# Kernel tuning notes

Hardware: AMD Instinct MI355X
Metric: run time of the kernel (lower is better)

## Reference

```python
import jax, jax.numpy as jnp
import numpy as np

DIM = 256      # in_channels == hidden_channels
INNER = 256    # heads * dim_head
HEADS = 4
DH = 64        # dim_head = hidden_channels // num_heads
EDGE_DIM = 512 # 2 * in_channels
FF = 1024      # 4 * dim ff expansion
DEPTH = 2
OUT = 1
N = 50000      # two stacked graphs of 25000 nodes
E = 100000
HALF = 25000


def setup_inputs() -> dict:
    key = jax.random.key(0)
    ks = iter(jax.random.split(key, 32))

    def lin(fan_in, fan_out):
        w = jax.random.normal(next(ks), (DEPTH, fan_in, fan_out), jnp.float32) * (1.0 / np.sqrt(fan_in))
        b = jnp.zeros((DEPTH, fan_out), jnp.float32)
        return w, b

    x = jax.random.normal(next(ks), (N, DIM), jnp.float32)
    edge_index = jax.random.randint(next(ks), (2, E), 0, HALF, dtype=jnp.int32)
    Wq, bq = lin(DIM, INNER)
    Wkv, bkv = lin(DIM, 2 * INNER)
    We, be = lin(EDGE_DIM, INNER)
    Wo, bo = lin(INNER, DIM)
    W1, b1 = lin(DIM, FF)
    W2, b2 = lin(FF, DIM)
    g_attn = jax.random.normal(next(ks), (DEPTH, 3 * DIM, 1), jnp.float32) * (1.0 / np.sqrt(3 * DIM))
    g_ff = jax.random.normal(next(ks), (DEPTH, 3 * DIM, 1), jnp.float32) * (1.0 / np.sqrt(3 * DIM))
    ln1_g = jnp.ones((DEPTH, DIM), jnp.float32); ln1_b = jnp.zeros((DEPTH, DIM), jnp.float32)
    ln2_g = jnp.ones((DEPTH, DIM), jnp.float32); ln2_b = jnp.zeros((DEPTH, DIM), jnp.float32)
    Wout = jax.random.normal(next(ks), (DIM, OUT), jnp.float32) * (1.0 / np.sqrt(DIM))
    bout = jnp.zeros((OUT,), jnp.float32)
    return dict(x=x, edge_index=edge_index, ln1_g=ln1_g, ln1_b=ln1_b, Wq=Wq, bq=bq,
                Wkv=Wkv, bkv=bkv, We=We, be=be, Wo=Wo, bo=bo, g_attn=g_attn,
                ln2_g=ln2_g, ln2_b=ln2_b, W1=W1, b1=b1, W2=W2, b2=b2, g_ff=g_ff,
                Wout=Wout, bout=bout)


def _layer_norm(x, g, b):
    mu = jnp.mean(x, axis=-1, keepdims=True)
    var = jnp.mean(jnp.square(x - mu), axis=-1, keepdims=True)
    return (x - mu) * jax.lax.rsqrt(var + 1e-5) * g + b


def _gated_residual(x, res, w):
    # gate = sigmoid(Linear_no_bias(cat(x, res, x - res)))
    gate = jax.nn.sigmoid(jnp.concatenate([x, res, x - res], axis=-1) @ w)  # [n,1]
    return x * gate + res * (1.0 - gate)


def _forward(x, edge_index, ln1_g, ln1_b, Wq, bq, Wkv, bkv, We, be, Wo, bo, g_attn,
             ln2_g, ln2_b, W1, b1, W2, b2, g_ff, Wout, bout):
    src, dst = edge_index[0], edge_index[1]
    # edge_attr = cat(x[src], x[dst]) as built in DeepGraphTransformer_mse.forward
    edge_attr = jnp.concatenate([x[src], x[dst]], axis=-1)  # [E, 2*DIM]
    nodes = x
    n = nodes.shape[0]
    scale = DH ** -0.5
    for l in range(DEPTH):
        xn = _layer_norm(nodes, ln1_g[l], ln1_b[l])
        q = xn @ Wq[l] + bq[l]                                   # [n, INNER]
        k, v = jnp.split(xn @ Wkv[l] + bkv[l], 2, axis=-1)       # [n, INNER] each
        e = edge_attr @ We[l] + be[l]                            # [E, INNER]
        qe = q[dst].reshape(-1, HEADS, DH)                       # [E,H,Dh]
        ke = (k[src] + e).reshape(-1, HEADS, DH)
        ve = (v[src] + e).reshape(-1, HEADS, DH)
        sim = jnp.einsum('ehd,ehd->eh', qe, ke) * scale          # [E,H]
        smax = jax.ops.segment_max(sim, dst, num_segments=n)     # [n,H] (-inf for empty)
        ez = jnp.exp(sim - smax[dst])
        denom = jax.ops.segment_sum(ez, dst, num_segments=n)
        attn = ez / denom[dst]                                   # softmax over incoming edges
        agg = jax.ops.segment_sum(attn[:, :, None] * ve, dst, num_segments=n)
        attn_out = agg.reshape(n, INNER) @ Wo[l] + bo[l]         # [n, DIM]
        nodes = _gated_residual(attn_out, nodes, g_attn[l])
        xn2 = _layer_norm(nodes, ln2_g[l], ln2_b[l])
        h = jax.nn.gelu(xn2 @ W1[l] + b1[l], approximate=False) @ W2[l] + b2[l]
        nodes = _gated_residual(h, nodes, g_ff[l])
    z = nodes @ Wout + bout                                      # [n, OUT]
    return z


def reference(x, edge_index, ln1_g, ln1_b, Wq, bq, Wkv, bkv, We, be, Wo, bo, g_attn,
              ln2_g, ln2_b, W1, b1, W2, b2, g_ff, Wout, bout):
    z = _forward(x, edge_index, ln1_g, ln1_b, Wq, bq, Wkv, bkv, We, be, Wo, bo, g_attn,
                 ln2_g, ln2_b, W1, b1, W2, b2, g_ff, Wout, bout)
    half = z.shape[0] // 2
    z_old, z_new = z[:half], z[half:]
    return (z_new.reshape(-1), z_old, z_new)
```

## Files before the change

kernel.cpp:

```cpp
#include <hip/hip_runtime.h>
#include <cmath>

#define N_NODES 50000
#define N_EDGES 100000
#define HALF_N  25000
#define DIM     256
#define NDEPTH  2
#define MAXDEG  64

#define WT_QKVE 0
#define WT_WO   524288
#define WT_W1   589824
#define WT_W2   851968
#define WT_LAYER 1114112

typedef __bf16 bf16;
typedef bf16 bf16x8 __attribute__((ext_vector_type(8)));
typedef bf16 bf16x4 __attribute__((ext_vector_type(4)));
typedef float f32x4 __attribute__((ext_vector_type(4)));

__device__ __forceinline__ float wave_sum(float v) {
  v += __shfl_xor(v, 1);
  v += __shfl_xor(v, 2);
  v += __shfl_xor(v, 4);
  v += __shfl_xor(v, 8);
  v += __shfl_xor(v, 16);
  v += __shfl_xor(v, 32);
  return v;
}

__global__ void ln0_kernel(const float* __restrict__ in, const float* __restrict__ g,
                           const float* __restrict__ b, bf16* __restrict__ A2) {
  int row = blockIdx.x * 4 + (threadIdx.x >> 6);
  if (row >= HALF_N) return;
  int lane = threadIdx.x & 63;
  float4 x = reinterpret_cast<const float4*>(in + (size_t)row * DIM)[lane];
  float mu = wave_sum(x.x + x.y + x.z + x.w) * (1.0f / DIM);
  float d0 = x.x - mu, d1 = x.y - mu, d2 = x.z - mu, d3 = x.w - mu;
  float var = wave_sum(d0*d0 + d1*d1 + d2*d2 + d3*d3) * (1.0f / DIM);
  float r = rsqrtf(var + 1e-5f);
  float4 gv = reinterpret_cast<const float4*>(g)[lane];
  float4 bv = reinterpret_cast<const float4*>(b)[lane];
  bf16x4 o;
  o[0] = (bf16)(d0 * r * gv.x + bv.x);
  o[1] = (bf16)(d1 * r * gv.y + bv.y);
  o[2] = (bf16)(d2 * r * gv.z + bv.z);
  o[3] = (bf16)(d3 * r * gv.w + bv.w);
  *reinterpret_cast<bf16x4*>(A2 + (size_t)row * 512 + lane * 4) = o;
}

template<int KK, int NJ>
__global__ __launch_bounds__(256) void gemm_nloop(
    const bf16* __restrict__ A, const bf16* __restrict__ Wp,
    const float* __restrict__ bias, bf16* __restrict__ C, int M) {
  __shared__ bf16x8 As[KK * 8];
  __shared__ bf16x8 Bs[1024];
  const int tid = threadIdx.x;
  const int lane = tid & 63, wv = tid >> 6;
  const int wr = wv >> 1, wc = wv & 1;
  const int lm = lane & 15, kb = (lane >> 4) & 3;
  const int row0 = blockIdx.x * 64;
#pragma unroll
  for (int i = 0; i < KK / 32; ++i) {
    int idx = tid + i * 256;
    int row = idx & 63, k8 = idx >> 6;
    int rga = row0 + row; if (rga >= M) rga = M - 1;
    As[idx] = *reinterpret_cast<const bf16x8*>(A + (size_t)rga * KK + k8 * 8);
  }
  const bf16x8* Wp8 = reinterpret_cast<const bf16x8*>(Wp);
  for (int jn = 0; jn < NJ; ++jn) {
    f32x4 acc[2][4] = {};
    for (int step = 0; step < KK / 64; ++step) {
      __syncthreads();
#pragma unroll
      for (int i = 0; i < 4; ++i) {
        int idx = tid + i * 256;
        Bs[idx] = Wp8[(size_t)jn * (KK * 16) + step * 1024 + idx];
      }
      __syncthreads();
#pragma unroll
      for (int ks = 0; ks < 2; ++ks) {
        bf16x8 af[2], bf[4];
#pragma unroll
        for (int mi = 0; mi < 2; ++mi)
          af[mi] = As[(step * 8 + ks * 4 + kb) * 64 + wr * 32 + mi * 16 + lm];
#pragma unroll
        for (int ni = 0; ni < 4; ++ni)
          bf[ni] = Bs[(ks * 4 + kb) * 128 + wc * 64 + ni * 16 + lm];
#pragma unroll
        for (int mi = 0; mi < 2; ++mi)
#pragma unroll
          for (int ni = 0; ni < 4; ++ni)
            acc[mi][ni] = __builtin_amdgcn_mfma_f32_16x16x32_bf16(af[mi], bf[ni], acc[mi][ni], 0, 0, 0);
      }
    }
    __syncthreads();
    bf16* Cs = (bf16*)Bs;
#pragma unroll
    for (int ni = 0; ni < 4; ++ni) {
      int c = wc * 64 + ni * 16 + lm;
      float bval = bias[jn * 128 + c];
#pragma unroll
      for (int mi = 0; mi < 2; ++mi)
#pragma unroll
        for (int e = 0; e < 4; ++e) {
          int r = wr * 32 + mi * 16 + kb * 4 + e;
          Cs[r * 128 + c] = (bf16)(acc[mi][ni][e] + bval);
        }
    }
    __syncthreads();
    bf16x8* C8 = reinterpret_cast<bf16x8*>(C);
    const bf16x8* Cs8 = (const bf16x8*)Bs;
#pragma unroll
    for (int i = 0; i < 4; ++i) {
      int idx = tid + i * 256;
      int row = idx >> 4, c8 = idx & 15;
      int grow = row0 + row;
      if (grow < M) C8[(size_t)grow * (NJ * 16) + jn * 16 + c8] = Cs8[row * 16 + c8];
    }
  }
}

__global__ __launch_bounds__(512) void ff_fused(
    const bf16* __restrict__ A, const bf16* __restrict__ W1p,
    const float* __restrict__ b1, const bf16* __restrict__ W2p,
    const float* __restrict__ b2, bf16* __restrict__ C, int M) {
  __shared__ bf16x8 Xs[2048];
  __shared__ bf16x8 Bs[2048];
  __shared__ bf16x8 Hs[1024];
  const int tid = threadIdx.x;
  const int lane = tid & 63, wv = tid >> 6;
  const int wr = wv >> 2, wc = wv & 3;
  const int lm = lane & 15, kb = (lane >> 4) & 3;
  const int row0 = blockIdx.x * 64;
#pragma unroll
  for (int i = 0; i < 4; ++i) {
    int idx = tid + i * 512;
    int row = idx & 63, k8 = idx >> 6;
    int rga = row0 + row; if (rga >= M) rga = M - 1;
    Xs[idx] = *reinterpret_cast<const bf16x8*>(A + (size_t)rga * 256 + k8 * 8);
  }
  const bf16x8* W1p8 = (const bf16x8*)W1p;
  const bf16x8* W2p8 = (const bf16x8*)W2p;
  f32x4 acc[2][4] = {};
  bf16* hsb = (bf16*)Hs;
  for (int j = 0; j < 8; ++j) {
    f32x4 acc1[2][2] = {};
#pragma unroll
    for (int half = 0; half < 2; ++half) {
      __syncthreads();
#pragma unroll
      for (int i = 0; i < 4; ++i) {
        int idx = tid + i * 512;
        Bs[idx] = W1p8[j * 4096 + half * 2048 + idx];
      }
      __syncthreads();
#pragma unroll
      for (int ks = 0; ks < 4; ++ks) {
        bf16x8 af[2], bf[2];
#pragma unroll
        for (int mi = 0; mi < 2; ++mi)
          af[mi] = Xs[(half * 16 + ks * 4 + kb) * 64 + wr * 32 + mi * 16 + lm];
#pragma unroll
        for (int ni = 0; ni < 2; ++ni)
          bf[ni] = Bs[(ks * 4 + kb) * 128 + wc * 32 + ni * 16 + lm];
#pragma unroll
        for (int mi = 0; mi < 2; ++mi)
#pragma unroll
          for (int ni = 0; ni < 2; ++ni)
            acc1[mi][ni] = __builtin_amdgcn_mfma_f32_16x16x32_bf16(af[mi], bf[ni], acc1[mi][ni], 0, 0, 0);
      }
    }
#pragma unroll
    for (int ni = 0; ni < 2; ++ni) {
      int c = wc * 32 + ni * 16 + lm;
      float bval = b1[j * 128 + c];
#pragma unroll
      for (int mi = 0; mi < 2; ++mi)
#pragma unroll
        for (int e = 0; e < 4; ++e) {
          int r = wr * 32 + mi * 16 + kb * 4 + e;
          float v = acc1[mi][ni][e] + bval;
          v = 0.5f * v * (1.0f + erff(v * 0.70710678118654752f));
          hsb[((c >> 3) * 64 + r) * 8 + (c & 7)] = (bf16)v;
        }
    }
#pragma unroll
    for (int h2 = 0; h2 < 2; ++h2) {
      __syncthreads();
#pragma unroll
      for (int i = 0; i < 4; ++i) {
        int idx = tid + i * 512;
        Bs[idx] = W2p8[j * 4096 + h2 * 2048 + idx];
      }
      __syncthreads();
#pragma unroll
      for (int ks = 0; ks < 2; ++ks) {
        bf16x8 af[2], bf[4];
#pragma unroll
        for (int mi = 0; mi < 2; ++mi)
          af[mi] = Hs[(h2 * 8 + ks * 4 + kb) * 64 + wr * 32 + mi * 16 + lm];
#pragma unroll
        for (int ni = 0; ni < 4; ++ni)
          bf[ni] = Bs[(ks * 4 + kb) * 256 + wc * 64 + ni * 16 + lm];
#pragma unroll
        for (int mi = 0; mi < 2; ++mi)
#pragma unroll
          for (int ni = 0; ni < 4; ++ni)
            acc[mi][ni] = __builtin_amdgcn_mfma_f32_16x16x32_bf16(af[mi], bf[ni], acc[mi][ni], 0, 0, 0);
      }
    }
  }
  __syncthreads();
  bf16* Cs = (bf16*)Bs;
#pragma unroll
  for (int ni = 0; ni < 4; ++ni) {
    int c = wc * 64 + ni * 16 + lm;
    float bval = b2[c];
#pragma unroll
    for (int mi = 0; mi < 2; ++mi)
#pragma unroll
      for (int e = 0; e < 4; ++e) {
        int r = wr * 32 + mi * 16 + kb * 4 + e;
        Cs[r * 256 + c] = (bf16)(acc[mi][ni][e] + bval);
      }
  }
  __syncthreads();
  bf16x8* C8 = (bf16x8*)C;
  const bf16x8* Cs8 = (const bf16x8*)Bs;
#pragma unroll
  for (int i = 0; i < 4; ++i) {
    int idx = tid + i * 512;
    int row = idx >> 5, c8 = idx & 31;
    int grow = row0 + row;
    if (grow < M) C8[(size_t)grow * 32 + c8] = Cs8[row * 32 + c8];
  }
}

__global__ void ell_build(const int* __restrict__ ei, int* __restrict__ deg,
                          int* __restrict__ ell) {
  int e = blockIdx.x * 256 + threadIdx.x;
  if (e >= N_EDGES) return;
  int s = ei[e], d = ei[N_EDGES + e];
  int pos = atomicAdd(&deg[d], 1);
  if (pos < MAXDEG) ell[d * MAXDEG + pos] = s;
}

__global__ void attn_gather(const int* __restrict__ deg, const int* __restrict__ ell,
                            const bf16* __restrict__ qkv, bf16* __restrict__ agg) {
  int d = blockIdx.x * 4 + (threadIdx.x >> 6);
  if (d >= HALF_N) return;
  int lane = threadIdx.x & 63;
  int cnt = deg[d]; if (cnt > MAXDEG) cnt = MAXDEG;
  const bf16* qr = qkv + (size_t)d * 1024;
  bf16x4 qb = *reinterpret_cast<const bf16x4*>(qr + lane * 4);
  float q0 = (float)qb[0], q1 = (float)qb[1], q2 = (float)qb[2], q3 = (float)qb[3];
  float m = -INFINITY, den = 0.0f, a0 = 0.0f, a1 = 0.0f, a2 = 0.0f, a3 = 0.0f;
  for (int i = 0; i < cnt; ++i) {
    int s = ell[d * MAXDEG + i];
    const bf16* kr = qkv + (size_t)s * 1024;
    bf16x4 kb4 = *reinterpret_cast<const bf16x4*>(kr + 256 + lane * 4);
    bf16x4 vb4 = *reinterpret_cast<const bf16x4*>(kr + 512 + lane * 4);
    float p = q0 * (float)kb4[0] + q1 * (float)kb4[1] +
              q2 * (float)kb4[2] + q3 * (float)kb4[3];
    p += __shfl_xor(p, 1); p += __shfl_xor(p, 2);
    p += __shfl_xor(p, 4); p += __shfl_xor(p, 8);
    float sim = p * 0.125f;
    float nm = fmaxf(m, sim);
    float sc = expf(m - nm);
    float w  = expf(sim - nm);
    den = den * sc + w;
    a0 = a0 * sc + w * (float)vb4[0];
    a1 = a1 * sc + w * (float)vb4[1];
    a2 = a2 * sc + w * (float)vb4[2];
    a3 = a3 * sc + w * (float)vb4[3];
    m = nm;
  }
  bf16x4 o;
  if (cnt > 0) {
    float inv = 1.0f / den;
    bf16x4 eb = *reinterpret_cast<const bf16x4*>(qr + 768 + lane * 4);
    o[0] = (bf16)(a0 * inv + (float)eb[0]);
    o[1] = (bf16)(a1 * inv + (float)eb[1]);
    o[2] = (bf16)(a2 * inv + (float)eb[2]);
    o[3] = (bf16)(a3 * inv + (float)eb[3]);
  } else {
    o[0] = (bf16)0.0f; o[1] = (bf16)0.0f; o[2] = (bf16)0.0f; o[3] = (bf16)0.0f;
  }
  *reinterpret_cast<bf16x4*>(agg + (size_t)d * DIM + lane * 4) = o;
}

template<int DO_LN, int DO_OUT>
__global__ void gr_ln(const bf16* __restrict__ xin, const float* __restrict__ fb,
                      float* __restrict__ nodes, const float* __restrict__ w,
                      const float* __restrict__ g, const float* __restrict__ b,
                      bf16* __restrict__ xn, int xn_stride, int ln_rows,
                      const float* __restrict__ Wout, const float* __restrict__ bout,
                      float* __restrict__ out, int rows, int xvr, int row_off) {
  int r = blockIdx.x * 4 + (threadIdx.x >> 6);
  if (r >= rows) return;
  int lane = threadIdx.x & 63;
  float x0, x1, x2, x3;
  if (r < xvr) {
    bf16x4 xb = *reinterpret_cast<const bf16x4*>(xin + (size_t)r * DIM + lane * 4);
    x0 = (float)xb[0]; x1 = (float)xb[1]; x2 = (float)xb[2]; x3 = (float)xb[3];
  } else {
    float4 f = reinterpret_cast<const float4*>(fb)[lane];
    x0 = f.x; x1 = f.y; x2 = f.z; x3 = f.w;
  }
  float4 rv = reinterpret_cast<const float4*>(nodes + (size_t)r * DIM)[lane];
  float4 w0 = reinterpret_cast<const float4*>(w)[lane];
  float4 w1 = reinterpret_cast<const float4*>(w + 256)[lane];
  float4 w2 = reinterpret_cast<const float4*>(w + 512)[lane];
  float p = x0 * (w0.x + w2.x) + rv.x * (w1.x - w2.x)
          + x1 * (w0.y + w2.y) + rv.y * (w1.y - w2.y)
          + x2 * (w0.z + w2.z) + rv.z * (w1.z - w2.z)
          + x3 * (w0.w + w2.w) + rv.w * (w1.w - w2.w);
  p = wave_sum(p);
  float gate = 1.0f / (1.0f + expf(-p));
  float n0 = x0 * gate + rv.x * (1.0f - gate);
  float n1 = x1 * gate + rv.y * (1.0f - gate);
  float n2 = x2 * gate + rv.z * (1.0f - gate);
  float n3 = x3 * gate + rv.w * (1.0f - gate);
  if (!DO_OUT) {
    float4 o; o.x = n0; o.y = n1; o.z = n2; o.w = n3;
    reinterpret_cast<float4*>(nodes + (size_t)r * DIM)[lane] = o;
  }
  if (DO_LN) {
    if (r < ln_rows) {
      float mu = wave_sum(n0 + n1 + n2 + n3) * (1.0f / DIM);
      float d0 = n0 - mu, d1 = n1 - mu, d2 = n2 - mu, d3 = n3 - mu;
      float var = wave_sum(d0*d0 + d1*d1 + d2*d2 + d3*d3) * (1.0f / DIM);
      float rs = rsqrtf(var + 1e-5f);
      float4 gv = reinterpret_cast<const float4*>(g)[lane];
      float4 bv = reinterpret_cast<const float4*>(b)[lane];
      bf16x4 o;
      o[0] = (bf16)(d0 * rs * gv.x + bv.x);
      o[1] = (bf16)(d1 * rs * gv.y + bv.y);
      o[2] = (bf16)(d2 * rs * gv.z + bv.z);
      o[3] = (bf16)(d3 * rs * gv.w + bv.w);
      *reinterpret_cast<bf16x4*>(xn + (size_t)r * xn_stride + lane * 4) = o;
    }
  }
  if (DO_OUT) {
    float4 wv = reinterpret_cast<const float4*>(Wout)[lane];
    float z = n0 * wv.x + n1 * wv.y + n2 * wv.z + n3 * wv.w;
    z = wave_sum(z);
    if (lane == 0) {
      z += bout[0];
      int gr = row_off + r;
      if (gr < HALF_N) {
        out[HALF_N + gr] = z;
      } else {
        int j = gr - HALF_N;
        out[j] = z;
        out[2 * HALF_N + j] = z;
      }
    }
  }
}

__global__ void prep_w(const float* __restrict__ Wq, const float* __restrict__ Wkv,
                       const float* __restrict__ We, const float* __restrict__ Wo,
                       const float* __restrict__ W1, const float* __restrict__ W2,
                       bf16* __restrict__ wt) {
  int idx = blockIdx.x * 256 + threadIdx.x;
  if (idx >= 2 * WT_LAYER) return;
  int l = idx / WT_LAYER, r = idx % WT_LAYER;
  float v;
  if (r < 524288) {
    int jn = r >> 16, t = r & 65535;
    int k8 = t >> 10, u = t & 1023, n = u >> 3, e = u & 7;
    int ncol = jn * 128 + n, k = k8 * 8 + e;
    if (ncol < 256) v = (k < 256) ? Wq[l * 65536 + k * 256 + ncol] : 0.0f;
    else if (ncol < 512) { int c = ncol - 256;
      v = (k < 256) ? Wkv[l * 131072 + k * 512 + c] : We[l * 131072 + (k - 256) * 256 + c]; }
    else if (ncol < 768) { int c = ncol - 512;
      v = (k < 256) ? Wkv[l * 131072 + k * 512 + 256 + c] : We[l * 131072 + (k - 256) * 256 + c]; }
    else { int c = ncol - 768;
      v = (k < 256) ? 0.0f : We[l * 131072 + k * 256 + c]; }
  } else if (r < 589824) {
    int rr = r - 524288;
    int jn = rr >> 15, t = rr & 32767;
    int k8 = t >> 10, u = t & 1023, n = u >> 3, e = u & 7;
    v = Wo[l * 65536 + (k8 * 8 + e) * 256 + jn * 128 + n];
  } else if (r < 851968) {
    int rr = r - 589824;
    int j = rr >> 15, t = rr & 32767;
    int k8 = t >> 10, u = t & 1023, n = u >> 3, e = u & 7;
    v = W1[l * 262144 + (k8 * 8 + e) * 1024 + j * 128 + n];
  } else {
    int rr = r - 851968;
    int j = rr >> 15, t = rr & 32767;
    int k8 = t >> 11, u = t & 2047, n = u >> 3, e = u & 7;
    v = W2[l * 262144 + (j * 128 + k8 * 8 + e) * 256 + n];
  }
  wt[idx] = (bf16)v;
}

__global__ void prep_bias(const float* __restrict__ bq, const float* __restrict__ bkv,
                          const float* __restrict__ be, float* __restrict__ biasq) {
  int i = blockIdx.x * 256 + threadIdx.x;
  if (i >= 2048) return;
  int l = i >> 10, n = i & 1023;
  float v;
  if (n < 256) v = bq[l * 256 + n];
  else if (n < 512) v = bkv[l * 512 + (n - 256)];
  else if (n < 768) v = bkv[l * 512 + 256 + (n - 512)];
  else v = be[l * 256 + (n - 768)];
  biasq[i] = v;
}

__global__ void prep_x(const float* __restrict__ x, bf16* __restrict__ A2) {
  int i = blockIdx.x * 256 + threadIdx.x;
  if (i >= HALF_N * 64) return;
  int row = i >> 6, c = i & 63;
  float4 v = reinterpret_cast<const float4*>(x)[i];
  bf16x4 o;
  o[0] = (bf16)v.x; o[1] = (bf16)v.y; o[2] = (bf16)v.z; o[3] = (bf16)v.w;
  *reinterpret_cast<bf16x4*>(A2 + (size_t)row * 512 + 256 + c * 4) = o;
}

extern "C" void kernel_launch(void* const* d_in, const int* in_sizes, int n_in,
                              void* d_out, int out_size, void* d_ws, size_t ws_size,
                              hipStream_t stream) {
  const float* x     = (const float*)d_in[0];
  const int*   ei    = (const int*)d_in[1];
  const float* ln1_g = (const float*)d_in[2];
  const float* ln1_b = (const float*)d_in[3];
  const float* Wq    = (const float*)d_in[4];
  const float* bq    = (const float*)d_in[5];
  const float* Wkv   = (const float*)d_in[6];
  const float* bkv   = (const float*)d_in[7];
  const float* We    = (const float*)d_in[8];
  const float* be    = (const float*)d_in[9];
  const float* Wo    = (const float*)d_in[10];
  const float* bo    = (const float*)d_in[11];
  const float* g_attn= (const float*)d_in[12];
  const float* ln2_g = (const float*)d_in[13];
  const float* ln2_b = (const float*)d_in[14];
  const float* W1    = (const float*)d_in[15];
  const float* b1    = (const float*)d_in[16];
  const float* W2    = (const float*)d_in[17];
  const float* b2    = (const float*)d_in[18];
  const float* g_ff  = (const float*)d_in[19];
  const float* Wout  = (const float*)d_in[20];
  const float* bout  = (const float*)d_in[21];
  float* out = (float*)d_out;

  char* base = (char*)d_ws;
  float* nodes   = (float*)base;  base += (size_t)N_NODES * DIM * 4;
  bf16*  A2      = (bf16*)base;   base += (size_t)HALF_N * 512 * 2;
  bf16*  xn_bf   = (bf16*)base;   base += (size_t)N_NODES * DIM * 2;
  bf16*  qkv     = (bf16*)base;   base += (size_t)HALF_N * 1024 * 2;
  bf16*  agg     = (bf16*)base;   base += (size_t)HALF_N * DIM * 2;
  bf16*  attn_o  = (bf16*)base;   base += (size_t)HALF_N * DIM * 2;
  bf16*  ffout   = (bf16*)base;   base += (size_t)N_NODES * DIM * 2;
  bf16*  wt      = (bf16*)base;   base += (size_t)2 * WT_LAYER * 2;
  float* biasq   = (float*)base;  base += 2048 * 4;
  int*   deg     = (int*)base;    base += HALF_N * 4;
  int*   ell     = (int*)base;    base += (size_t)HALF_N * MAXDEG * 4;

  hipMemcpyAsync(nodes, x, (size_t)N_NODES * DIM * sizeof(float),
                 hipMemcpyDeviceToDevice, stream);
  prep_w<<<(2 * WT_LAYER + 255) / 256, 256, 0, stream>>>(Wq, Wkv, We, Wo, W1, W2, wt);
  prep_bias<<<8, 256, 0, stream>>>(bq, bkv, be, biasq);
  prep_x<<<(HALF_N * 64 + 255) / 256, 256, 0, stream>>>(x, A2);
  hipMemsetAsync(deg, 0, HALF_N * sizeof(int), stream);
  ell_build<<<(N_EDGES + 255) / 256, 256, 0, stream>>>(ei, deg, ell);

  const int GP_H = (HALF_N + 63) / 64;
  const int GP_N = (N_NODES + 63) / 64;

  for (int l = 0; l < NDEPTH; ++l) {
    const bf16* wl = wt + (size_t)l * WT_LAYER;
    if (l == 0)
      ln0_kernel<<<(HALF_N + 3) / 4, 256, 0, stream>>>(x, ln1_g, ln1_b, A2);
    gemm_nloop<512, 8><<<GP_H, 256, 0, stream>>>(A2, wl + WT_QKVE, biasq + l * 1024, qkv, HALF_N);
    attn_gather<<<(HALF_N + 3) / 4, 256, 0, stream>>>(deg, ell, qkv, agg);
    gemm_nloop<256, 2><<<GP_H, 256, 0, stream>>>(agg, wl + WT_WO, bo + l * DIM, attn_o, HALF_N);
    gr_ln<1, 0><<<(N_NODES + 3) / 4, 256, 0, stream>>>(
        attn_o, bo + l * DIM, nodes, g_attn + l * 768,
        ln2_g + l * DIM, ln2_b + l * DIM, xn_bf, DIM, N_NODES,
        nullptr, nullptr, nullptr, N_NODES, HALF_N, 0);
    ff_fused<<<GP_N, 512, 0, stream>>>(xn_bf, wl + WT_W1, b1 + l * 1024,
                                       wl + WT_W2, b2 + l * DIM, ffout, N_NODES);
    if (l < NDEPTH - 1) {
      gr_ln<1, 0><<<(N_NODES + 3) / 4, 256, 0, stream>>>(
          ffout, nullptr, nodes, g_ff + l * 768,
          ln1_g + (l + 1) * DIM, ln1_b + (l + 1) * DIM, A2, 512, HALF_N,
          nullptr, nullptr, nullptr, N_NODES, N_NODES, 0);
    } else {
      gr_ln<0, 1><<<(N_NODES + 3) / 4, 256, 0, stream>>>(
          ffout, nullptr, nodes, g_ff + l * 768,
          nullptr, nullptr, nullptr, 0, 0,
          Wout, bout, out, N_NODES, N_NODES, 0);
    }
  }
}
```

Measured before the change: 553.2 us.

## Fuse gated-residual and layernorm epilogues into GEMMs, prefetch weights, interleave K/V

Fuses the attention output projection with its gated residual and LayerNorm, and the FF block with its gated residual plus either the next LayerNorm or the final output projection. This removes the intermediate bf16 buffers and the separate residual kernels. Weight tiles are now prefetched into registers one step ahead in all GEMMs, and the exact erf GELU is replaced by a polynomial approximation. K and V are interleaved so attention loads both with one 16-byte read, and fast exp intrinsics are used. In exchange the code carries more register pressure and larger LDS footprints, and the approximations introduce small numeric differences.

Result: slower. 594.5 us (+7.5%).

```diff
diff --git a/kernel.cpp b/kernel.cpp
--- a/kernel.cpp
+++ b/kernel.cpp
@@ -27,6 +27,17 @@
   v += __shfl_xor(v, 16);
   v += __shfl_xor(v, 32);
   return v;
+}
+
+__device__ __forceinline__ float fast_gelu(float v) {
+  float ax = fabsf(v) * 0.70710678118654752f;
+  float t = __builtin_amdgcn_rcpf(fmaf(0.3275911f, ax, 1.0f));
+  float p = t * fmaf(t, fmaf(t, fmaf(t, fmaf(t, 1.061405429f, -1.453152027f),
+                                     1.421413741f), -0.284496736f), 0.254829592f);
+  float e = __expf(-ax * ax);
+  float erfv = fmaf(-p, e, 1.0f);
+  float ph = copysignf(erfv, v);
+  return 0.5f * v * (1.0f + ph);
 }
 
 __global__ void ln0_kernel(const float* __restrict__ in, const float* __restrict__ g,
@@ -50,9 +61,10 @@
 }
 
 template<int KK, int NJ>
-__global__ __launch_bounds__(256) void gemm_nloop(
+__global__ __launch_bounds__(256, 2) void gemm_nloop(
     const bf16* __restrict__ A, const bf16* __restrict__ Wp,
     const float* __restrict__ bias, bf16* __restrict__ C, int M) {
+  constexpr int STEPS = KK / 64;
   __shared__ bf16x8 As[KK * 8];
   __shared__ bf16x8 Bs[1024];
   const int tid = threadIdx.x;
@@ -68,30 +80,37 @@
     As[idx] = *reinterpret_cast<const bf16x8*>(A + (size_t)rga * KK + k8 * 8);
   }
   const bf16x8* Wp8 = reinterpret_cast<const bf16x8*>(Wp);
+  bf16x8 pf[4];
+  auto ldpf = [&](int p) {
+    int jn = p / STEPS, st = p % STEPS;
+    const bf16x8* src = Wp8 + (size_t)jn * (KK * 16) + st * 1024;
+#pragma unroll
+    for (int i = 0; i < 4; ++i) pf[i] = src[tid + i * 256];
+  };
+  ldpf(0);
   for (int jn = 0; jn < NJ; ++jn) {
     f32x4 acc[2][4] = {};
-    for (int step = 0; step < KK / 64; ++step) {
+    for (int st = 0; st < STEPS; ++st) {
       __syncthreads();
 #pragma unroll
-      for (int i = 0; i < 4; ++i) {
-        int idx = tid + i * 256;
-        Bs[idx] = Wp8[(size_t)jn * (KK * 16) + step * 1024 + idx];
-      }
+      for (int i = 0; i < 4; ++i) Bs[tid + i * 256] = pf[i];
       __syncthreads();
+      int p = jn * STEPS + st + 1;
+      if (p < NJ * STEPS) ldpf(p);
 #pragma unroll
       for (int ks = 0; ks < 2; ++ks) {
-        bf16x8 af[2], bf[4];
+        bf16x8 af[2], bfr[4];
 #pragma unroll
         for (int mi = 0; mi < 2; ++mi)
-          af[mi] = As[(step * 8 + ks * 4 + kb) * 64 + wr * 32 + mi * 16 + lm];
+          af[mi] = As[(st * 8 + ks * 4 + kb) * 64 + wr * 32 + mi * 16 + lm];
 #pragma unroll
         for (int ni = 0; ni < 4; ++ni)
-          bf[ni] = Bs[(ks * 4 + kb) * 128 + wc * 64 + ni * 16 + lm];
+          bfr[ni] = Bs[(ks * 4 + kb) * 128 + wc * 64 + ni * 16 + lm];
 #pragma unroll
         for (int mi = 0; mi < 2; ++mi)
 #pragma unroll
           for (int ni = 0; ni < 4; ++ni)
-            acc[mi][ni] = __builtin_amdgcn_mfma_f32_16x16x32_bf16(af[mi], bf[ni], acc[mi][ni], 0, 0, 0);
+            acc[mi][ni] = __builtin_amdgcn_mfma_f32_16x16x32_bf16(af[mi], bfr[ni], acc[mi][ni], 0, 0, 0);
       }
     }
     __syncthreads();
@@ -121,10 +140,148 @@
   }
 }
 
-__global__ __launch_bounds__(512) void ff_fused(
+__global__ __launch_bounds__(256, 2) void wo_fused(
+    const bf16* __restrict__ A, const bf16* __restrict__ Wp,
+    const float* __restrict__ bo, const float* __restrict__ gattn,
+    const float* __restrict__ ln2g, const float* __restrict__ ln2b,
+    float* __restrict__ nodes, bf16* __restrict__ xn, int M) {
+  __shared__ bf16x8 As[2048];
+  __shared__ bf16x8 Bs[1024];
+  __shared__ bf16 Cs[64 * 256];
+  const int tid = threadIdx.x;
+  const int lane = tid & 63, wv = tid >> 6;
+  const int wr = wv >> 1, wc = wv & 1;
+  const int lm = lane & 15, kb = (lane >> 4) & 3;
+  const int row0 = blockIdx.x * 64;
+#pragma unroll
+  for (int i = 0; i < 8; ++i) {
+    int idx = tid + i * 256;
+    int row = idx & 63, k8 = idx >> 6;
+    int rga = row0 + row; if (rga >= M) rga = M - 1;
+    As[idx] = *reinterpret_cast<const bf16x8*>(A + (size_t)rga * 256 + k8 * 8);
+  }
+  const bf16x8* Wp8 = (const bf16x8*)Wp;
+  bf16x8 pf[4];
+  auto ldpf = [&](int p) {
+    const bf16x8* src = Wp8 + (p >> 2) * 4096 + (p & 3) * 1024;
+#pragma unroll
+    for (int i = 0; i < 4; ++i) pf[i] = src[tid + i * 256];
+  };
+  ldpf(0);
+  for (int jn = 0; jn < 2; ++jn) {
+    f32x4 acc[2][4] = {};
+    for (int st = 0; st < 4; ++st) {
+      __syncthreads();
+#pragma unroll
+      for (int i = 0; i < 4; ++i) Bs[tid + i * 256] = pf[i];
+      __syncthreads();
+      int p = jn * 4 + st + 1;
+      if (p < 8) ldpf(p);
+#pragma unroll
+      for (int ks = 0; ks < 2; ++ks) {
+        bf16x8 af[2], bfr[4];
+#pragma unroll
+        for (int mi = 0; mi < 2; ++mi)
+          af[mi] = As[(st * 8 + ks * 4 + kb) * 64 + wr * 32 + mi * 16 + lm];
+#pragma unroll
+        for (int ni = 0; ni < 4; ++ni)
+          bfr[ni] = Bs[(ks * 4 + kb) * 128 + wc * 64 + ni * 16 + lm];
+#pragma unroll
+        for (int mi = 0; mi < 2; ++mi)
+#pragma unroll
+          for (int ni = 0; ni < 4; ++ni)
+            acc[mi][ni] = __builtin_amdgcn_mfma_f32_16x16x32_bf16(af[mi], bfr[ni], acc[mi][ni], 0, 0, 0);
+      }
+    }
+#pragma unroll
+    for (int ni = 0; ni < 4; ++ni) {
+      int cfull = jn * 128 + wc * 64 + ni * 16 + lm;
+      float bval = bo[cfull];
+#pragma unroll
+      for (int mi = 0; mi < 2; ++mi)
+#pragma unroll
+        for (int e = 0; e < 4; ++e) {
+          int r = wr * 32 + mi * 16 + kb * 4 + e;
+          int ch = (cfull >> 3) ^ (r & 7);
+          Cs[r * 256 + ch * 8 + (cfull & 7)] = (bf16)(acc[mi][ni][e] + bval);
+        }
+    }
+  }
+  __syncthreads();
+  int r = tid >> 2, grp = tid & 3;
+  int grow = row0 + r;
+  if (grow < M) {
+    float xv[64], rv[64];
+#pragma unroll
+    for (int i = 0; i < 8; ++i) {
+      int ch = (grp * 8 + i) ^ (r & 7);
+      bf16x8 c8 = *reinterpret_cast<const bf16x8*>(Cs + r * 256 + ch * 8);
+#pragma unroll
+      for (int e = 0; e < 8; ++e) xv[i * 8 + e] = (float)c8[e];
+    }
+    const float* nrow = nodes + (size_t)grow * 256 + grp * 64;
+#pragma unroll
+    for (int i = 0; i < 16; ++i) {
+      float4 f = reinterpret_cast<const float4*>(nrow)[i];
+      rv[i*4] = f.x; rv[i*4+1] = f.y; rv[i*4+2] = f.z; rv[i*4+3] = f.w;
+    }
+    float dot = 0.0f;
+    const float* gw = gattn + grp * 64;
+#pragma unroll
+    for (int i = 0; i < 16; ++i) {
+      float4 w0 = reinterpret_cast<const float4*>(gw)[i];
+      float4 w1 = reinterpret_cast<const float4*>(gw + 256)[i];
+      float4 w2 = reinterpret_cast<const float4*>(gw + 512)[i];
+      int c = i * 4;
+      dot += xv[c]   * (w0.x + w2.x) + rv[c]   * (w1.x - w2.x);
+      dot += xv[c+1] * (w0.y + w2.y) + rv[c+1] * (w1.y - w2.y);
+      dot += xv[c+2] * (w0.z + w2.z) + rv[c+2] * (w1.z - w2.z);
+      dot += xv[c+3] * (w0.w + w2.w) + rv[c+3] * (w1.w - w2.w);
+    }
+    dot += __shfl_xor(dot, 1); dot += __shfl_xor(dot, 2);
+    float gate = 1.0f / (1.0f + __expf(-dot));
+#pragma unroll
+    for (int c = 0; c < 64; ++c) xv[c] = fmaf(xv[c] - rv[c], gate, rv[c]);
+    float4* nw = (float4*)(nodes + (size_t)grow * 256 + grp * 64);
+#pragma unroll
+    for (int i = 0; i < 16; ++i) {
+      float4 o; o.x = xv[i*4]; o.y = xv[i*4+1]; o.z = xv[i*4+2]; o.w = xv[i*4+3];
+      nw[i] = o;
+    }
+    float s = 0.0f;
+#pragma unroll
+    for (int c = 0; c < 64; ++c) s += xv[c];
+    s += __shfl_xor(s, 1); s += __shfl_xor(s, 2);
+    float mu = s * (1.0f / DIM);
+    float vs = 0.0f;
+#pragma unroll
+    for (int c = 0; c < 64; ++c) { float d = xv[c] - mu; vs += d * d; }
+    vs += __shfl_xor(vs, 1); vs += __shfl_xor(vs, 2);
+    float rs = rsqrtf(vs * (1.0f / DIM) + 1e-5f);
+    const float* lg = ln2g + grp * 64;
+    const float* lb = ln2b + grp * 64;
+#pragma unroll
+    for (int i = 0; i < 8; ++i) {
+      bf16x8 o;
+#pragma unroll
+      for (int e = 0; e < 8; ++e) {
+        int c = i * 8 + e;
+        o[e] = (bf16)((xv[c] - mu) * rs * lg[c] + lb[c]);
+      }
+      *reinterpret_cast<bf16x8*>(xn + (size_t)grow * 256 + grp * 64 + i * 8) = o;
+    }
+  }
+}
+
+template<int LAST>
+__global__ __launch_bounds__(512, 4) void ff_fused(
     const bf16* __restrict__ A, const bf16* __restrict__ W1p,
     const float* __restrict__ b1, const bf16* __restrict__ W2p,
-    const float* __restrict__ b2, bf16* __restrict__ C, int M) {
+    const float* __restrict__ b2, float* __restrict__ nodes,
+    const float* __restrict__ gff, const float* __restrict__ ln1g,
+    const float* __restrict__ ln1b, bf16* __restrict__ A2,
+    const float* __restrict__ Wout, const float* __restrict__ bout,
+    float* __restrict__ out, int M) {
   __shared__ bf16x8 Xs[2048];
   __shared__ bf16x8 Bs[2048];
   __shared__ bf16x8 Hs[1024];
@@ -142,6 +299,13 @@
   }
   const bf16x8* W1p8 = (const bf16x8*)W1p;
   const bf16x8* W2p8 = (const bf16x8*)W2p;
+  bf16x8 pf[4];
+  auto ldpf = [&](int p) {
+    const bf16x8* src = (((p & 3) < 2) ? W1p8 : W2p8) + ((p >> 2) * 4096 + (p & 1) * 2048);
+#pragma unroll
+    for (int i = 0; i < 4; ++i) pf[i] = src[tid + i * 512];
+  };
+  ldpf(0);
   f32x4 acc[2][4] = {};
   bf16* hsb = (bf16*)Hs;
   for (int j = 0; j < 8; ++j) {
@@ -150,25 +314,23 @@
     for (int half = 0; half < 2; ++half) {
       __syncthreads();
 #pragma unroll
-      for (int i = 0; i < 4; ++i) {
-        int idx = tid + i * 512;
-        Bs[idx] = W1p8[j * 4096 + half * 2048 + idx];
-      }
+      for (int i = 0; i < 4; ++i) Bs[tid + i * 512] = pf[i];
       __syncthreads();
+      ldpf(j * 4 + half + 1);
 #pragma unroll
       for (int ks = 0; ks < 4; ++ks) {
-        bf16x8 af[2], bf[2];
+        bf16x8 af[2], bfr[2];
 #pragma unroll
         for (int mi = 0; mi < 2; ++mi)
           af[mi] = Xs[(half * 16 + ks * 4 + kb) * 64 + wr * 32 + mi * 16 + lm];
 #pragma unroll
         for (int ni = 0; ni < 2; ++ni)
-          bf[ni] = Bs[(ks * 4 + kb) * 128 + wc * 32 + ni * 16 + lm];
+          bfr[ni] = Bs[(ks * 4 + kb) * 128 + wc * 32 + ni * 16 + lm];
 #pragma unroll
         for (int mi = 0; mi < 2; ++mi)
 #pragma unroll
           for (int ni = 0; ni < 2; ++ni)
-            acc1[mi][ni] = __builtin_amdgcn_mfma_f32_16x16x32_bf16(af[mi], bf[ni], acc1[mi][ni], 0, 0, 0);
+            acc1[mi][ni] = __builtin_amdgcn_mfma_f32_16x16x32_bf16(af[mi], bfr[ni], acc1[mi][ni], 0, 0, 0);
       }
     }
 #pragma unroll
@@ -180,8 +342,7 @@
 #pragma unroll
         for (int e = 0; e < 4; ++e) {
           int r = wr * 32 + mi * 16 + kb * 4 + e;
-          float v = acc1[mi][ni][e] + bval;
-          v = 0.5f * v * (1.0f + erff(v * 0.70710678118654752f));
+          float v = fast_gelu(acc1[mi][ni][e] + bval);
           hsb[((c >> 3) * 64 + r) * 8 + (c & 7)] = (bf16)v;
         }
     }
@@ -189,25 +350,24 @@
     for (int h2 = 0; h2 < 2; ++h2) {
       __syncthreads();
 #pragma unroll
-      for (int i = 0; i < 4; ++i) {
-        int idx = tid + i * 512;
-        Bs[idx] = W2p8[j * 4096 + h2 * 2048 + idx];
-      }
+      for (int i = 0; i < 4; ++i) Bs[tid + i * 512] = pf[i];
       __syncthreads();
+      int p = j * 4 + 2 + h2 + 1;
+      if (p < 32) ldpf(p);
 #pragma unroll
       for (int ks = 0; ks < 2; ++ks) {
-        bf16x8 af[2], bf[4];
+        bf16x8 af[2], bfr[4];
 #pragma unroll
         for (int mi = 0; mi < 2; ++mi)
           af[mi] = Hs[(h2 * 8 + ks * 4 + kb) * 64 + wr * 32 + mi * 16 + lm];
 #pragma unroll
         for (int ni = 0; ni < 4; ++ni)
-          bf[ni] = Bs[(ks * 4 + kb) * 256 + wc * 64 + ni * 16 + lm];
+          bfr[ni] = Bs[(ks * 4 + kb) * 256 + wc * 64 + ni * 16 + lm];
 #pragma unroll
         for (int mi = 0; mi < 2; ++mi)
 #pragma unroll
           for (int ni = 0; ni < 4; ++ni)
-            acc[mi][ni] = __builtin_amdgcn_mfma_f32_16x16x32_bf16(af[mi], bf[ni], acc[mi][ni], 0, 0, 0);
+            acc[mi][ni] = __builtin_amdgcn_mfma_f32_16x16x32_bf16(af[mi], bfr[ni], acc[mi][ni], 0, 0, 0);
       }
     }
   }
@@ -222,18 +382,95 @@
 #pragma unroll
       for (int e = 0; e < 4; ++e) {
         int r = wr * 32 + mi * 16 + kb * 4 + e;
-        Cs[r * 256 + c] = (bf16)(acc[mi][ni][e] + bval);
+        int ch = (c >> 3) ^ (r & 7);
+        Cs[r * 256 + ch * 8 + (c & 7)] = (bf16)(acc[mi][ni][e] + bval);
       }
   }
   __syncthreads();
-  bf16x8* C8 = (bf16x8*)C;
-  const bf16x8* Cs8 = (const bf16x8*)Bs;
-#pragma unroll
-  for (int i = 0; i < 4; ++i) {
-    int idx = tid + i * 512;
-    int row = idx >> 5, c8 = idx & 31;
-    int grow = row0 + row;
-    if (grow < M) C8[(size_t)grow * 32 + c8] = Cs8[row * 32 + c8];
+  int r = tid >> 3, grp = tid & 7;
+  int grow = row0 + r;
+  if (grow < M) {
+    float xv[32], rv[32];
+#pragma unroll
+    for (int i = 0; i < 4; ++i) {
+      int ch = (grp * 4 + i) ^ (r & 7);
+      bf16x8 c8 = *reinterpret_cast<const bf16x8*>(Cs + r * 256 + ch * 8);
+#pragma unroll
+      for (int e = 0; e < 8; ++e) xv[i * 8 + e] = (float)c8[e];
+    }
+    const float* nrow = nodes + (size_t)grow * 256 + grp * 32;
+#pragma unroll
+    for (int i = 0; i < 8; ++i) {
+      float4 f = reinterpret_cast<const float4*>(nrow)[i];
+      rv[i*4] = f.x; rv[i*4+1] = f.y; rv[i*4+2] = f.z; rv[i*4+3] = f.w;
+    }
+    float dot = 0.0f, dx = 0.0f, dr = 0.0f;
+    const float* gw = gff + grp * 32;
+#pragma unroll
+    for (int i = 0; i < 8; ++i) {
+      float4 w0 = reinterpret_cast<const float4*>(gw)[i];
+      float4 w1 = reinterpret_cast<const float4*>(gw + 256)[i];
+      float4 w2 = reinterpret_cast<const float4*>(gw + 512)[i];
+      int c = i * 4;
+      dot += xv[c]   * (w0.x + w2.x) + rv[c]   * (w1.x - w2.x);
+      dot += xv[c+1] * (w0.y + w2.y) + rv[c+1] * (w1.y - w2.y);
+      dot += xv[c+2] * (w0.z + w2.z) + rv[c+2] * (w1.z - w2.z);
+      dot += xv[c+3] * (w0.w + w2.w) + rv[c+3] * (w1.w - w2.w);
+      if (LAST) {
+        float4 wo4 = reinterpret_cast<const float4*>(Wout + grp * 32)[i];
+        dx += xv[c]*wo4.x + xv[c+1]*wo4.y + xv[c+2]*wo4.z + xv[c+3]*wo4.w;
+        dr += rv[c]*wo4.x + rv[c+1]*wo4.y + rv[c+2]*wo4.z + rv[c+3]*wo4.w;
+      }
+    }
+    dot += __shfl_xor(dot, 1); dot += __shfl_xor(dot, 2); dot += __shfl_xor(dot, 4);
+    float gate = 1.0f / (1.0f + __expf(-dot));
+    if (LAST) {
+      dx += __shfl_xor(dx, 1); dx += __shfl_xor(dx, 2); dx += __shfl_xor(dx, 4);
+      dr += __shfl_xor(dr, 1); dr += __shfl_xor(dr, 2); dr += __shfl_xor(dr, 4);
+      if (grp == 0) {
+        float z = gate * dx + (1.0f - gate) * dr + bout[0];
+        if (grow < HALF_N) {
+          out[HALF_N + grow] = z;
+        } else {
+          int jj = grow - HALF_N;
+          out[jj] = z;
+          out[2 * HALF_N + jj] = z;
+        }
+      }
+    } else {
+#pragma unroll
+      for (int c = 0; c < 32; ++c) xv[c] = fmaf(xv[c] - rv[c], gate, rv[c]);
+      float4* nw = (float4*)(nodes + (size_t)grow * 256 + grp * 32);
+#pragma unroll
+      for (int i = 0; i < 8; ++i) {
+        float4 o; o.x = xv[i*4]; o.y = xv[i*4+1]; o.z = xv[i*4+2]; o.w = xv[i*4+3];
+        nw[i] = o;
+      }
+      if (grow < HALF_N) {
+        float s = 0.0f;
+#pragma unroll
+        for (int c = 0; c < 32; ++c) s += xv[c];
+        s += __shfl_xor(s, 1); s += __shfl_xor(s, 2); s += __shfl_xor(s, 4);
+        float mu = s * (1.0f / DIM);
+        float vs = 0.0f;
+#pragma unroll
+        for (int c = 0; c < 32; ++c) { float d = xv[c] - mu; vs += d * d; }
+        vs += __shfl_xor(vs, 1); vs += __shfl_xor(vs, 2); vs += __shfl_xor(vs, 4);
+        float rs = rsqrtf(vs * (1.0f / DIM) + 1e-5f);
+        const float* lg = ln1g + grp * 32;
+        const float* lb = ln1b + grp * 32;
+#pragma unroll
+        for (int i = 0; i < 4; ++i) {
+          bf16x8 o;
+#pragma unroll
+          for (int e = 0; e < 8; ++e) {
+            int c = i * 8 + e;
+            o[e] = (bf16)((xv[c] - mu) * rs * lg[c] + lb[c]);
+          }
+          *reinterpret_cast<bf16x8*>(A2 + (size_t)grow * 512 + grp * 32 + i * 8) = o;
+        }
+      }
+    }
   }
 }
 
@@ -258,22 +495,20 @@
   float m = -INFINITY, den = 0.0f, a0 = 0.0f, a1 = 0.0f, a2 = 0.0f, a3 = 0.0f;
   for (int i = 0; i < cnt; ++i) {
     int s = ell[d * MAXDEG + i];
-    const bf16* kr = qkv + (size_t)s * 1024;
-    bf16x4 kb4 = *reinterpret_cast<const bf16x4*>(kr + 256 + lane * 4);
-    bf16x4 vb4 = *reinterpret_cast<const bf16x4*>(kr + 512 + lane * 4);
-    float p = q0 * (float)kb4[0] + q1 * (float)kb4[1] +
-              q2 * (float)kb4[2] + q3 * (float)kb4[3];
+    bf16x8 kv8 = *reinterpret_cast<const bf16x8*>(qkv + (size_t)s * 1024 + 256 + lane * 8);
+    float p = q0 * (float)kv8[0] + q1 * (float)kv8[1] +
+              q2 * (float)kv8[2] + q3 * (float)kv8[3];
     p += __shfl_xor(p, 1); p += __shfl_xor(p, 2);
     p += __shfl_xor(p, 4); p += __shfl_xor(p, 8);
     float sim = p * 0.125f;
     float nm = fmaxf(m, sim);
-    float sc = expf(m - nm);
-    float w  = expf(sim - nm);
+    float sc = __expf(m - nm);
+    float w  = __expf(sim - nm);
     den = den * sc + w;
-    a0 = a0 * sc + w * (float)vb4[0];
-    a1 = a1 * sc + w * (float)vb4[1];
-    a2 = a2 * sc + w * (float)vb4[2];
-    a3 = a3 * sc + w * (float)vb4[3];
+    a0 = a0 * sc + w * (float)kv8[4];
+    a1 = a1 * sc + w * (float)kv8[5];
+    a2 = a2 * sc + w * (float)kv8[6];
+    a3 = a3 * sc + w * (float)kv8[7];
     m = nm;
   }
   bf16x4 o;
@@ -295,8 +530,7 @@
                       float* __restrict__ nodes, const float* __restrict__ w,
                       const float* __restrict__ g, const float* __restrict__ b,
                       bf16* __restrict__ xn, int xn_stride, int ln_rows,
-                      const float* __restrict__ Wout, const float* __restrict__ bout,
-                      float* __restrict__ out, int rows, int xvr, int row_off) {
+                      int rows, int xvr) {
   int r = blockIdx.x * 4 + (threadIdx.x >> 6);
   if (r >= rows) return;
   int lane = threadIdx.x & 63;
@@ -317,46 +551,26 @@
           + x2 * (w0.z + w2.z) + rv.z * (w1.z - w2.z)
           + x3 * (w0.w + w2.w) + rv.w * (w1.w - w2.w);
   p = wave_sum(p);
-  float gate = 1.0f / (1.0f + expf(-p));
+  float gate = 1.0f / (1.0f + __expf(-p));
   float n0 = x0 * gate + rv.x * (1.0f - gate);
   float n1 = x1 * gate + rv.y * (1.0f - gate);
   float n2 = x2 * gate + rv.z * (1.0f - gate);
   float n3 = x3 * gate + rv.w * (1.0f - gate);
-  if (!DO_OUT) {
-    float4 o; o.x = n0; o.y = n1; o.z = n2; o.w = n3;
-    reinterpret_cast<float4*>(nodes + (size_t)r * DIM)[lane] = o;
-  }
-  if (DO_LN) {
-    if (r < ln_rows) {
-      float mu = wave_sum(n0 + n1 + n2 + n3) * (1.0f / DIM);
-      float d0 = n0 - mu, d1 = n1 - mu, d2 = n2 - mu, d3 = n3 - mu;
-      float var = wave_sum(d0*d0 + d1*d1 + d2*d2 + d3*d3) * (1.0f / DIM);
-      float rs = rsqrtf(var + 1e-5f);
-      float4 gv = reinterpret_cast<const float4*>(g)[lane];
-      float4 bv = reinterpret_cast<const float4*>(b)[lane];
-      bf16x4 o;
-      o[0] = (bf16)(d0 * rs * gv.x + bv.x);
-      o[1] = (bf16)(d1 * rs * gv.y + bv.y);
-      o[2] = (bf16)(d2 * rs * gv.z + bv.z);
-      o[3] = (bf16)(d3 * rs * gv.w + bv.w);
-      *reinterpret_cast<bf16x4*>(xn + (size_t)r * xn_stride + lane * 4) = o;
-    }
-  }
-  if (DO_OUT) {
-    float4 wv = reinterpret_cast<const float4*>(Wout)[lane];
-    float z = n0 * wv.x + n1 * wv.y + n2 * wv.z + n3 * wv.w;
-    z = wave_sum(z);
-    if (lane == 0) {
-      z += bout[0];
-      int gr = row_off + r;
-      if (gr < HALF_N) {
-        out[HALF_N + gr] = z;
-      } else {
-        int j = gr - HALF_N;
-        out[j] = z;
-        out[2 * HALF_N + j] = z;
-      }
-    }
+  float4 o; o.x = n0; o.y = n1; o.z = n2; o.w = n3;
+  reinterpret_cast<float4*>(nodes + (size_t)r * DIM)[lane] = o;
+  if (DO_LN && r < ln_rows) {
+    float mu = wave_sum(n0 + n1 + n2 + n3) * (1.0f / DIM);
+    float d0 = n0 - mu, d1 = n1 - mu, d2 = n2 - mu, d3 = n3 - mu;
+    float var = wave_sum(d0*d0 + d1*d1 + d2*d2 + d3*d3) * (1.0f / DIM);
+    float rs = rsqrtf(var + 1e-5f);
+    float4 gv = reinterpret_cast<const float4*>(g)[lane];
+    float4 bv = reinterpret_cast<const float4*>(b)[lane];
+    bf16x4 ob;
+    ob[0] = (bf16)(d0 * rs * gv.x + bv.x);
+    ob[1] = (bf16)(d1 * rs * gv.y + bv.y);
+    ob[2] = (bf16)(d2 * rs * gv.z + bv.z);
+    ob[3] = (bf16)(d3 * rs * gv.w + bv.w);
+    *reinterpret_cast<bf16x4*>(xn + (size_t)r * xn_stride + lane * 4) = ob;
   }
 }
 
@@ -372,13 +586,18 @@
     int jn = r >> 16, t = r & 65535;
     int k8 = t >> 10, u = t & 1023, n = u >> 3, e = u & 7;
     int ncol = jn * 128 + n, k = k8 * 8 + e;
-    if (ncol < 256) v = (k < 256) ? Wq[l * 65536 + k * 256 + ncol] : 0.0f;
-    else if (ncol < 512) { int c = ncol - 256;
-      v = (k < 256) ? Wkv[l * 131072 + k * 512 + c] : We[l * 131072 + (k - 256) * 256 + c]; }
-    else if (ncol < 768) { int c = ncol - 512;
-      v = (k < 256) ? Wkv[l * 131072 + k * 512 + 256 + c] : We[l * 131072 + (k - 256) * 256 + c]; }
-    else { int c = ncol - 768;
-      v = (k < 256) ? 0.0f : We[l * 131072 + k * 256 + c]; }
+    if (ncol < 256) {
+      v = (k < 256) ? Wq[l * 65536 + k * 256 + ncol] : 0.0f;
+    } else if (ncol < 768) {
+      int u2 = ncol - 256;
+      int c = (u2 >> 3) * 4 + (u2 & 3);
+      int half = (u2 >> 2) & 1;
+      if (k < 256) v = Wkv[l * 131072 + k * 512 + half * 256 + c];
+      else         v = We[l * 131072 + (k - 256) * 256 + c];
+    } else {
+      int c = ncol - 768;
+      v = (k < 256) ? 0.0f : We[l * 131072 + k * 256 + c];
+    }
   } else if (r < 589824) {
     int rr = r - 524288;
     int jn = rr >> 15, t = rr & 32767;
@@ -405,9 +624,12 @@
   int l = i >> 10, n = i & 1023;
   float v;
   if (n < 256) v = bq[l * 256 + n];
-  else if (n < 512) v = bkv[l * 512 + (n - 256)];
-  else if (n < 768) v = bkv[l * 512 + 256 + (n - 512)];
-  else v = be[l * 256 + (n - 768)];
+  else if (n < 768) {
+    int u2 = n - 256;
+    int c = (u2 >> 3) * 4 + (u2 & 3);
+    int half = (u2 >> 2) & 1;
+    v = bkv[l * 512 + half * 256 + c];
+  } else v = be[l * 256 + (n - 768)];
   biasq[i] = v;
 }
 
@@ -454,8 +676,6 @@
   bf16*  xn_bf   = (bf16*)base;   base += (size_t)N_NODES * DIM * 2;
   bf16*  qkv     = (bf16*)base;   base += (size_t)HALF_N * 1024 * 2;
   bf16*  agg     = (bf16*)base;   base += (size_t)HALF_N * DIM * 2;
-  bf16*  attn_o  = (bf16*)base;   base += (size_t)HALF_N * DIM * 2;
-  bf16*  ffout   = (bf16*)base;   base += (size_t)N_NODES * DIM * 2;
   bf16*  wt      = (bf16*)base;   base += (size_t)2 * WT_LAYER * 2;
   float* biasq   = (float*)base;  base += 2048 * 4;
   int*   deg     = (int*)base;    base += HALF_N * 4;
@@ -478,23 +698,23 @@
       ln0_kernel<<<(HALF_N + 3) / 4, 256, 0, stream>>>(x, ln1_g, ln1_b, A2);
     gemm_nloop<512, 8><<<GP_H, 256, 0, stream>>>(A2, wl + WT_QKVE, biasq + l * 1024, qkv, HALF_N);
     attn_gather<<<(HALF_N + 3) / 4, 256, 0, stream>>>(deg, ell, qkv, agg);
-    gemm_nloop<256, 2><<<GP_H, 256, 0, stream>>>(agg, wl + WT_WO, bo + l * DIM, attn_o, HALF_N);
-    gr_ln<1, 0><<<(N_NODES + 3) / 4, 256, 0, stream>>>(
-        attn_o, bo + l * DIM, nodes, g_attn + l * 768,
-        ln2_g + l * DIM, ln2_b + l * DIM, xn_bf, DIM, N_NODES,
-        nullptr, nullptr, nullptr, N_NODES, HALF_N, 0);
-    ff_fused<<<GP_N, 512, 0, stream>>>(xn_bf, wl + WT_W1, b1 + l * 1024,
-                                       wl + WT_W2, b2 + l * DIM, ffout, N_NODES);
+    wo_fused<<<GP_H, 256, 0, stream>>>(agg, wl + WT_WO, bo + l * DIM,
+                                       g_attn + l * 768, ln2_g + l * DIM, ln2_b + l * DIM,
+                                       nodes, xn_bf, HALF_N);
+    gr_ln<1, 0><<<(HALF_N + 3) / 4, 256, 0, stream>>>(
+        nullptr, bo + l * DIM, nodes + (size_t)HALF_N * DIM, g_attn + l * 768,
+        ln2_g + l * DIM, ln2_b + l * DIM, xn_bf + (size_t)HALF_N * DIM, DIM, HALF_N,
+        HALF_N, 0);
     if (l < NDEPTH - 1) {
-      gr_ln<1, 0><<<(N_NODES + 3) / 4, 256, 0, stream>>>(
-          ffout, nullptr, nodes, g_ff + l * 768,
-          ln1_g + (l + 1) * DIM, ln1_b + (l + 1) * DIM, A2, 512, HALF_N,
-          nullptr, nullptr, nullptr, N_NODES, N_NODES, 0);
+      ff_fused<0><<<GP_N, 512, 0, stream>>>(
+          xn_bf, wl + WT_W1, b1 + l * 1024, wl + WT_W2, b2 + l * DIM,
+          nodes, g_ff + l * 768, ln1_g + (l + 1) * DIM, ln1_b + (l + 1) * DIM, A2,
+          nullptr, nullptr, nullptr, N_NODES);
     } else {
-      gr_ln<0, 1><<<(N_NODES + 3) / 4, 256, 0, stream>>>(
-          ffout, nullptr, nodes, g_ff + l * 768,
-          nullptr, nullptr, nullptr, 0, 0,
-          Wout, bout, out, N_NODES, N_NODES, 0);
-    }
-  }
-}
+      ff_fused<1><<<GP_N, 512, 0, stream>>>(
+          xn_bf, wl + WT_W1, b1 + l * 1024, wl + WT_W2, b2 + l * DIM,
+          nodes, g_ff + l * 768, nullptr, nullptr, nullptr,
+          Wout, bout, out, N_NODES);
+    }
+  }
+}
```
